# Performance work log

Hardware: AMD Instinct MI355X
Metric: run time of the kernel (lower is better)

The kernel has to match this reference:

```python
import jax, jax.numpy as jnp
import numpy as np

R = 8          # number of areas of interest (regions)
C = 32         # n_channels_per_region
NPR = 128      # neurons per region (contiguous layout)
RKEEP = 6      # R - int(R * r_ratio), r_ratio = 0.25
HID = 1024     # hidden_size
NLAT = 160     # sum of n_lat over regions (20 * 8)


def setup_inputs() -> dict:
    key = jax.random.key(0)
    ks = jax.random.split(key, 8)
    B, T = 32, 1024
    N = R * NPR
    spikes = jax.random.normal(ks[0], (B, T, N), jnp.float32)
    # per-(session,area) Linear weights, stacked over regions: [R, C, NPR]
    W_area = jax.random.normal(ks[1], (R, C, NPR), jnp.float32) / np.sqrt(NPR)
    b_area = jax.random.normal(ks[2], (R, C), jnp.float32) * 0.01
    U_W = jax.random.normal(ks[3], (HID, R * C), jnp.float32) / np.sqrt(R * C)
    U_b = jnp.zeros((HID,), jnp.float32)
    V_W = jax.random.normal(ks[4], (NLAT, HID), jnp.float32) / np.sqrt(HID)
    V_b = jnp.zeros((NLAT,), jnp.float32)
    # per-sample random region permutation (MAE-style mask): argsort of noise
    noise = jax.random.uniform(ks[5], (B, R))
    ids_shuffle = jnp.argsort(noise, axis=1).astype(jnp.int32)
    return dict(spikes=spikes, W_area=W_area, b_area=b_area,
                U_W=U_W, U_b=U_b, V_W=V_W, V_b=V_b, ids_shuffle=ids_shuffle)


def reference(spikes, W_area, b_area, U_W, U_b, V_W, V_b, ids_shuffle):
    B, T, N = spikes.shape
    # Stitcher: per-area gather -> small Linear -> scatter into region slots.
    # Regions are contiguous (neuron n belongs to region n // NPR), so the
    # torch.where gather is a static reshape; preprocess_X is identity
    # (smoothing=False, halfbin_X=0).
    x = spikes.reshape(B, T, R, NPR)
    region_emb = jnp.einsum('btrn,rcn->btrc', x, W_area) + b_area  # [B,T,R,C]
    # random_mask over regions: keep RKEEP regions per sample
    ids_keep = ids_shuffle[:, :RKEEP]                 # [B, RKEEP]
    ids_restore = jnp.argsort(ids_shuffle, axis=1)    # [B, R]
    x_masked = jnp.take_along_axis(region_emb, ids_keep[:, None, :, None], axis=2)
    # append zero mask tokens and restore original region order
    mask_tok = jnp.zeros((B, T, R - RKEEP, C), region_emb.dtype)
    x_full = jnp.concatenate([x_masked, mask_tok], axis=2)        # [B,T,R,C]
    x_rest = jnp.take_along_axis(x_full, ids_restore[:, None, :, None], axis=2)
    h = x_rest.reshape(B, T, R * C)
    u = h @ U_W.T + U_b                                # [B,T,HID]
    return u @ V_W.T + V_b                             # [B,T,NLAT]
```

## Files before the change

### kernel.cpp

```cpp
#include <hip/hip_runtime.h>
#include <hip/hip_bf16.h>


typedef float f32x4 __attribute__((ext_vector_type(4)));
typedef __bf16 bf16x8 __attribute__((ext_vector_type(8)));

__global__ __launch_bounds__(256) void pa_kernel(const float* __restrict__ V_W,
                                                 const float* __restrict__ U_W,
                                                 float* __restrict__ M_part) {
    const int rc = threadIdx.x;
    const int lq = blockIdx.x >> 2;
    const int ck = blockIdx.x & 3;
    const int l0 = lq * 4;
    const int h0 = ck * 256;
    float a0 = 0.f, a1 = 0.f, a2 = 0.f, a3 = 0.f;
#pragma unroll 4
    for (int hh = 0; hh < 256; ++hh) {
        const int h = h0 + hh;
        const float u = U_W[h * 256 + rc];
        a0 += V_W[(l0 + 0) * 1024 + h] * u;
        a1 += V_W[(l0 + 1) * 1024 + h] * u;
        a2 += V_W[(l0 + 2) * 1024 + h] * u;
        a3 += V_W[(l0 + 3) * 1024 + h] * u;
    }
    float* dst = M_part + (size_t)ck * 160 * 256;
    dst[(l0 + 0) * 256 + rc] = a0;
    dst[(l0 + 1) * 256 + rc] = a1;
    dst[(l0 + 2) * 256 + rc] = a2;
    dst[(l0 + 3) * 256 + rc] = a3;
}

__global__ __launch_bounds__(256) void pb_kernel(const float* __restrict__ M_part,
                                                 const float* __restrict__ W_area,
                                                 const float* __restrict__ b_area,
                                                 const float* __restrict__ V_W,
                                                 const float* __restrict__ U_b,
                                                 const float* __restrict__ V_b,
                                                 __bf16* __restrict__ F,
                                                 float* __restrict__ bias_area,
                                                 float* __restrict__ bias0) {
    const int l = blockIdx.x;
    const int tid = threadIdx.x;
    __shared__ float Mrow[256];
    __shared__ float red[256];

    float m = 0.f;
#pragma unroll
    for (int p = 0; p < 4; ++p) m += M_part[(size_t)(p * 160 + l) * 256 + tid];
    Mrow[tid] = m;

    float p0 = 0.f;
#pragma unroll
    for (int hh = 0; hh < 4; ++hh) {
        const int h = tid + hh * 256;
        p0 += V_W[(size_t)l * 1024 + h] * U_b[h];
    }
    red[tid] = p0;
    __syncthreads();

#pragma unroll
    for (int p = 0; p < 4; ++p) {
        const int rn = tid + p * 256;
        const int r = rn >> 7, n = rn & 127;
        float acc = 0.f;
#pragma unroll 8
        for (int c = 0; c < 32; ++c)
            acc += Mrow[r * 32 + c] * W_area[((r * 32 + c) << 7) + n];
        F[(size_t)l * 1024 + rn] = (__bf16)acc;
    }

    if (tid < 8) {
        const int r = tid;
        float acc = 0.f;
        for (int c = 0; c < 32; ++c) acc += Mrow[r * 32 + c] * b_area[r * 32 + c];
        bias_area[l * 8 + r] = acc;
    }

    for (int off = 128; off > 0; off >>= 1) {
        __syncthreads();
        if (tid < off) red[tid] += red[tid + off];
    }
    if (tid == 0) bias0[l] = V_b[l] + red[0];
}

__global__ __launch_bounds__(256, 1) void main_kernel(const float* __restrict__ spikes,
                                                      const int* __restrict__ ids,
                                                      const __bf16* __restrict__ F,
                                                      const float* __restrict__ bias_area,
                                                      const float* __restrict__ bias0,
                                                      float* __restrict__ out) {
    const int tid = threadIdx.x;
    const int lane = tid & 63;
    const int wave = tid >> 6;
    const int s = lane & 15;
    const int q = lane >> 4;
    const int blk = blockIdx.x;
    const int b = blk >> 3;
    const int tok0 = blk * 128 + wave * 32;

    int rj[6];
#pragma unroll
    for (int j = 0; j < 6; ++j) rj[j] = ids[b * 8 + j];

    f32x4 acc[2][10];
#pragma unroll
    for (int mt = 0; mt < 2; ++mt)
#pragma unroll
        for (int nt = 0; nt < 10; ++nt) acc[mt][nt] = (f32x4){0.f, 0.f, 0.f, 0.f};

#pragma unroll 1
    for (int j = 0; j < 6; ++j) {
        const int colbase = rj[j] * 128;
        float4 rawA[2][4][2];
#pragma unroll
        for (int mt = 0; mt < 2; ++mt) {
            const float* rowp =
                spikes + (size_t)(tok0 + mt * 16 + s) * 1024 + colbase + q * 8;
#pragma unroll
            for (int kk = 0; kk < 4; ++kk) {
                rawA[mt][kk][0] = *(const float4*)(rowp + kk * 32);
                rawA[mt][kk][1] = *(const float4*)(rowp + kk * 32 + 4);
            }
        }
#pragma unroll
        for (int kk = 0; kk < 4; ++kk) {
            const int col = colbase + kk * 32 + q * 8;
            bf16x8 bf[10];
#pragma unroll
            for (int nt = 0; nt < 10; ++nt)
                bf[nt] = *(const bf16x8*)(F + (size_t)(nt * 16 + s) * 1024 + col);
#pragma unroll
            for (int mt = 0; mt < 2; ++mt) {
                const float4 lo = rawA[mt][kk][0];
                const float4 hi = rawA[mt][kk][1];
                bf16x8 af;
                af[0] = (__bf16)lo.x; af[1] = (__bf16)lo.y;
                af[2] = (__bf16)lo.z; af[3] = (__bf16)lo.w;
                af[4] = (__bf16)hi.x; af[5] = (__bf16)hi.y;
                af[6] = (__bf16)hi.z; af[7] = (__bf16)hi.w;
#pragma unroll
                for (int nt = 0; nt < 10; ++nt)
                    acc[mt][nt] = __builtin_amdgcn_mfma_f32_16x16x32_bf16(
                        af, bf[nt], acc[mt][nt], 0, 0, 0);
            }
        }
    }

#pragma unroll
    for (int nt = 0; nt < 10; ++nt) {
        const int l = nt * 16 + s;
        float bias = bias0[l];
#pragma unroll
        for (int j = 0; j < 6; ++j) bias += bias_area[l * 8 + rj[j]];
#pragma unroll
        for (int mt = 0; mt < 2; ++mt) {
            const int tk = tok0 + mt * 16 + q * 4;
#pragma unroll
            for (int i = 0; i < 4; ++i)
                out[(size_t)(tk + i) * 160 + l] = acc[mt][nt][i] + bias;
        }
    }
}

extern "C" void kernel_launch(void* const* d_in, const int* in_sizes, int n_in,
                              void* d_out, int out_size, void* d_ws, size_t ws_size,
                              hipStream_t stream) {
    (void)in_sizes; (void)n_in; (void)out_size; (void)ws_size;
    const float* spikes = (const float*)d_in[0];
    const float* W_area = (const float*)d_in[1];
    const float* b_area = (const float*)d_in[2];
    const float* U_W    = (const float*)d_in[3];
    const float* U_b    = (const float*)d_in[4];
    const float* V_W    = (const float*)d_in[5];
    const float* V_b    = (const float*)d_in[6];
    const int*   ids    = (const int*)d_in[7];
    float* out = (float*)d_out;

    char* ws = (char*)d_ws;
    float*  M_part    = (float*)ws;
    __bf16* F         = (__bf16*)(ws + 655360);
    float*  bias_area = (float*)(ws + 983040);
    float*  bias0     = (float*)(ws + 988160);

    pa_kernel<<<160, 256, 0, stream>>>(V_W, U_W, M_part);
    pb_kernel<<<160, 256, 0, stream>>>(M_part, W_area, b_area, V_W, U_b, V_b,
                                       F, bias_area, bias0);
    main_kernel<<<256, 256, 0, stream>>>(spikes, ids, F, bias_area, bias0, out);
}
```

Baseline: 266.4 us.

## Split work finer across blocks in all three kernels to raise occupancy

The main GEMM kernel now assigns each wave a 16-token tile and half of the 160 outputs, launching 1024 blocks with higher occupancy bounds instead of 256 single-occupancy blocks. The precompute kernels split the K reduction 16 ways and the F construction 4 ways per output row to launch more blocks. This targets latency-bound underutilization of the GPU, at the cost of reloading spike rows for each output half and more partial-sum traffic.

```diff
diff --git a/kernel.cpp b/kernel.cpp
--- a/kernel.cpp
+++ b/kernel.cpp
@@ -5,17 +5,19 @@
 typedef float f32x4 __attribute__((ext_vector_type(4)));
 typedef __bf16 bf16x8 __attribute__((ext_vector_type(8)));
 
+#define KSPLIT 16
+
 __global__ __launch_bounds__(256) void pa_kernel(const float* __restrict__ V_W,
                                                  const float* __restrict__ U_W,
                                                  float* __restrict__ M_part) {
     const int rc = threadIdx.x;
-    const int lq = blockIdx.x >> 2;
-    const int ck = blockIdx.x & 3;
+    const int lq = blockIdx.x >> 4;
+    const int ck = blockIdx.x & 15;
     const int l0 = lq * 4;
-    const int h0 = ck * 256;
+    const int h0 = ck * 64;
     float a0 = 0.f, a1 = 0.f, a2 = 0.f, a3 = 0.f;
-#pragma unroll 4
-    for (int hh = 0; hh < 256; ++hh) {
+#pragma unroll 8
+    for (int hh = 0; hh < 64; ++hh) {
         const int h = h0 + hh;
         const float u = U_W[h * 256 + rc];
         a0 += V_W[(l0 + 0) * 1024 + h] * u;
@@ -39,14 +41,15 @@
                                                  __bf16* __restrict__ F,
                                                  float* __restrict__ bias_area,
                                                  float* __restrict__ bias0) {
-    const int l = blockIdx.x;
+    const int l = blockIdx.x >> 2;
+    const int p4 = blockIdx.x & 3;
     const int tid = threadIdx.x;
     __shared__ float Mrow[256];
     __shared__ float red[256];
 
     float m = 0.f;
 #pragma unroll
-    for (int p = 0; p < 4; ++p) m += M_part[(size_t)(p * 160 + l) * 256 + tid];
+    for (int p = 0; p < KSPLIT; ++p) m += M_part[(size_t)(p * 160 + l) * 256 + tid];
     Mrow[tid] = m;
 
     float p0 = 0.f;
@@ -58,32 +61,32 @@
     red[tid] = p0;
     __syncthreads();
 
-#pragma unroll
-    for (int p = 0; p < 4; ++p) {
-        const int rn = tid + p * 256;
+    {
+        const int rn = p4 * 256 + tid;
         const int r = rn >> 7, n = rn & 127;
         float acc = 0.f;
-#pragma unroll 8
+#pragma unroll
         for (int c = 0; c < 32; ++c)
             acc += Mrow[r * 32 + c] * W_area[((r * 32 + c) << 7) + n];
         F[(size_t)l * 1024 + rn] = (__bf16)acc;
     }
 
-    if (tid < 8) {
-        const int r = tid;
-        float acc = 0.f;
-        for (int c = 0; c < 32; ++c) acc += Mrow[r * 32 + c] * b_area[r * 32 + c];
-        bias_area[l * 8 + r] = acc;
+    if (p4 == 0) {
+        if (tid < 8) {
+            const int r = tid;
+            float acc = 0.f;
+            for (int c = 0; c < 32; ++c) acc += Mrow[r * 32 + c] * b_area[r * 32 + c];
+            bias_area[l * 8 + r] = acc;
+        }
+        for (int off = 128; off > 0; off >>= 1) {
+            __syncthreads();
+            if (tid < off) red[tid] += red[tid + off];
+        }
+        if (tid == 0) bias0[l] = V_b[l] + red[0];
     }
-
-    for (int off = 128; off > 0; off >>= 1) {
-        __syncthreads();
-        if (tid < off) red[tid] += red[tid + off];
-    }
-    if (tid == 0) bias0[l] = V_b[l] + red[0];
 }
 
-__global__ __launch_bounds__(256, 1) void main_kernel(const float* __restrict__ spikes,
+__global__ __launch_bounds__(256, 4) void main_kernel(const float* __restrict__ spikes,
                                                       const int* __restrict__ ids,
                                                       const __bf16* __restrict__ F,
                                                       const float* __restrict__ bias_area,
@@ -94,71 +97,64 @@
     const int wave = tid >> 6;
     const int s = lane & 15;
     const int q = lane >> 4;
-    const int blk = blockIdx.x;
-    const int b = blk >> 3;
-    const int tok0 = blk * 128 + wave * 32;
+    const int half = wave & 1;
+    const int tt = blockIdx.x * 2 + (wave >> 1);
+    const int tok0 = tt * 16;
+    const int b = tok0 >> 10;
 
     int rj[6];
 #pragma unroll
     for (int j = 0; j < 6; ++j) rj[j] = ids[b * 8 + j];
 
-    f32x4 acc[2][10];
+    f32x4 acc[5];
 #pragma unroll
-    for (int mt = 0; mt < 2; ++mt)
-#pragma unroll
-        for (int nt = 0; nt < 10; ++nt) acc[mt][nt] = (f32x4){0.f, 0.f, 0.f, 0.f};
+    for (int nt = 0; nt < 5; ++nt) acc[nt] = (f32x4){0.f, 0.f, 0.f, 0.f};
+
+    const __bf16* Fh = F + (size_t)(half * 80 + s) * 1024;
 
 #pragma unroll 1
     for (int j = 0; j < 6; ++j) {
         const int colbase = rj[j] * 128;
-        float4 rawA[2][4][2];
-#pragma unroll
-        for (int mt = 0; mt < 2; ++mt) {
-            const float* rowp =
-                spikes + (size_t)(tok0 + mt * 16 + s) * 1024 + colbase + q * 8;
+        float4 rawA[4][2];
+        {
+            const float* rowp = spikes + (size_t)(tok0 + s) * 1024 + colbase + q * 8;
 #pragma unroll
             for (int kk = 0; kk < 4; ++kk) {
-                rawA[mt][kk][0] = *(const float4*)(rowp + kk * 32);
-                rawA[mt][kk][1] = *(const float4*)(rowp + kk * 32 + 4);
+                rawA[kk][0] = *(const float4*)(rowp + kk * 32);
+                rawA[kk][1] = *(const float4*)(rowp + kk * 32 + 4);
             }
         }
 #pragma unroll
         for (int kk = 0; kk < 4; ++kk) {
             const int col = colbase + kk * 32 + q * 8;
-            bf16x8 bf[10];
+            bf16x8 bf[5];
 #pragma unroll
-            for (int nt = 0; nt < 10; ++nt)
-                bf[nt] = *(const bf16x8*)(F + (size_t)(nt * 16 + s) * 1024 + col);
+            for (int nt = 0; nt < 5; ++nt)
+                bf[nt] = *(const bf16x8*)(Fh + (size_t)nt * 16 * 1024 + col);
+            const float4 lo = rawA[kk][0];
+            const float4 hi = rawA[kk][1];
+            bf16x8 af;
+            af[0] = (__bf16)lo.x; af[1] = (__bf16)lo.y;
+            af[2] = (__bf16)lo.z; af[3] = (__bf16)lo.w;
+            af[4] = (__bf16)hi.x; af[5] = (__bf16)hi.y;
+            af[6] = (__bf16)hi.z; af[7] = (__bf16)hi.w;
 #pragma unroll
-            for (int mt = 0; mt < 2; ++mt) {
-                const float4 lo = rawA[mt][kk][0];
-                const float4 hi = rawA[mt][kk][1];
-                bf16x8 af;
-                af[0] = (__bf16)lo.x; af[1] = (__bf16)lo.y;
-                af[2] = (__bf16)lo.z; af[3] = (__bf16)lo.w;
-                af[4] = (__bf16)hi.x; af[5] = (__bf16)hi.y;
-                af[6] = (__bf16)hi.z; af[7] = (__bf16)hi.w;
-#pragma unroll
-                for (int nt = 0; nt < 10; ++nt)
-                    acc[mt][nt] = __builtin_amdgcn_mfma_f32_16x16x32_bf16(
-                        af, bf[nt], acc[mt][nt], 0, 0, 0);
-            }
+            for (int nt = 0; nt < 5; ++nt)
+                acc[nt] = __builtin_amdgcn_mfma_f32_16x16x32_bf16(
+                    af, bf[nt], acc[nt], 0, 0, 0);
         }
     }
 
 #pragma unroll
-    for (int nt = 0; nt < 10; ++nt) {
-        const int l = nt * 16 + s;
+    for (int nt = 0; nt < 5; ++nt) {
+        const int l = half * 80 + nt * 16 + s;
         float bias = bias0[l];
 #pragma unroll
         for (int j = 0; j < 6; ++j) bias += bias_area[l * 8 + rj[j]];
+        const int tk = tok0 + q * 4;
 #pragma unroll
-        for (int mt = 0; mt < 2; ++mt) {
-            const int tk = tok0 + mt * 16 + q * 4;
-#pragma unroll
-            for (int i = 0; i < 4; ++i)
-                out[(size_t)(tk + i) * 160 + l] = acc[mt][nt][i] + bias;
-        }
+        for (int i = 0; i < 4; ++i)
+            out[(size_t)(tk + i) * 160 + l] = acc[nt][i] + bias;
     }
 }
 
@@ -178,12 +174,12 @@
 
     char* ws = (char*)d_ws;
     float*  M_part    = (float*)ws;
-    __bf16* F         = (__bf16*)(ws + 655360);
-    float*  bias_area = (float*)(ws + 983040);
-    float*  bias0     = (float*)(ws + 988160);
+    __bf16* F         = (__bf16*)(ws + 2621440);
+    float*  bias_area = (float*)(ws + 2949120);
+    float*  bias0     = (float*)(ws + 2954240);
 
-    pa_kernel<<<160, 256, 0, stream>>>(V_W, U_W, M_part);
-    pb_kernel<<<160, 256, 0, stream>>>(M_part, W_area, b_area, V_W, U_b, V_b,
+    pa_kernel<<<640, 256, 0, stream>>>(V_W, U_W, M_part);
+    pb_kernel<<<640, 256, 0, stream>>>(M_part, W_area, b_area, V_W, U_b, V_b,
                                        F, bias_area, bias0);
-    main_kernel<<<256, 256, 0, stream>>>(spikes, ids, F, bias_area, bias0, out);
+    main_kernel<<<1024, 256, 0, stream>>>(spikes, ids, F, bias_area, bias0, out);
 }
```

Result: slower. 274.8 us (+3.1%).
